# Performance work log

Hardware: AMD Instinct MI355X
Metric: run time of the kernel (lower is better)

## Reference

```python
import jax, jax.numpy as jnp
import numpy as np

N_NODES = 50000
N_EDGES = 500000
D_FEAT = 128


def setup_inputs() -> dict:
    key = jax.random.key(0)
    k1, k2, k3 = jax.random.split(key, 3)
    r = jax.random.normal(k1, (N_NODES, D_FEAT), dtype=jnp.float32)
    e = jax.random.normal(k2, (N_EDGES, D_FEAT), dtype=jnp.float32)
    a = jax.random.randint(k3, (N_EDGES, 2), 0, N_NODES, dtype=jnp.int64)
    return {"r": r, "e": e, "a": a}


def reference(r, e, a):
    # message: gather source/target node features along edges, scale by edge feats
    rij = r[a[:, 0]] * e  # [E, D] messages src -> dst
    rji = r[a[:, 1]] * e  # [E, D] messages dst -> src
    # aggregate: scatter_add into node dimension (fixed num_segments for jit)
    out = jax.ops.segment_sum(rij, a[:, 1], num_segments=r.shape[0])
    out = out + jax.ops.segment_sum(rji, a[:, 0], num_segments=r.shape[0])
    return out  # [N, D]
```

## Files before the change

kernel.cpp:

```cpp
#include <hip/hip_runtime.h>
#include <hip/hip_fp16.h>


#define D_FEAT 128
#define SCAN_TILE 1024

__device__ inline unsigned pack_h2(float a, float b) {
    __half2 h;
    h.x = __float2half_rn(a);
    h.y = __float2half_rn(b);
    return *reinterpret_cast<unsigned*>(&h);
}
__device__ inline float2 unpack_h2(unsigned u) {
    __half2 h = *reinterpret_cast<__half2*>(&u);
    return __half22float2(h);
}

__device__ inline unsigned bf16pack2(float a, float b) {
    unsigned ua = __float_as_uint(a), ub = __float_as_uint(b);
    ua += 0x7fffu + ((ua >> 16) & 1u);
    ub += 0x7fffu + ((ub >> 16) & 1u);
    return ((ua >> 16) & 0xffffu) | (ub & 0xffff0000u);
}

__global__ void hist_kernel(const int* __restrict__ a, int* __restrict__ deg,
                            int n_elems) {
    int i = blockIdx.x * blockDim.x + threadIdx.x;
    if (i < n_elems) atomicAdd(&deg[a[i]], 1);
}

__global__ void scanA_kernel(const int* __restrict__ deg, int* __restrict__ bsum,
                             int n) {
    __shared__ int wsum[16];
    int t = threadIdx.x, lane = t & 63, w = t >> 6;
    int i = blockIdx.x * SCAN_TILE + t;
    int v = (i < n) ? deg[i] : 0;
    #pragma unroll
    for (int off = 32; off > 0; off >>= 1) v += __shfl_down(v, off, 64);
    if (lane == 0) wsum[w] = v;
    __syncthreads();
    if (t == 0) {
        int s = 0;
        #pragma unroll
        for (int k = 0; k < 16; ++k) s += wsum[k];
        bsum[blockIdx.x] = s;
    }
}

__global__ void scanB_kernel(int* __restrict__ bsum, int* __restrict__ bbase,
                             int* __restrict__ offs, int nblk, int n) {
    if (threadIdx.x == 0) {
        int run = 0;
        for (int b = 0; b < nblk; ++b) {
            bbase[b] = run;
            run += bsum[b];
        }
        offs[n] = run;
    }
}

__global__ void scanC_kernel(int* __restrict__ deg, int* __restrict__ offs,
                             const int* __restrict__ bbase, int n) {
    __shared__ int wsum[16];
    int t = threadIdx.x, lane = t & 63, w = t >> 6;
    int i = blockIdx.x * SCAN_TILE + t;
    int v = (i < n) ? deg[i] : 0;
    int x = v;
    #pragma unroll
    for (int off = 1; off < 64; off <<= 1) {
        int y = __shfl_up(x, off, 64);
        if (lane >= off) x += y;
    }
    if (lane == 63) wsum[w] = x;
    __syncthreads();
    if (w == 0 && lane < 16) {
        int s = wsum[lane];
        #pragma unroll
        for (int off = 1; off < 16; off <<= 1) {
            int y = __shfl_up(s, off, 64);
            if (lane >= off) s += y;
        }
        wsum[lane] = s;
    }
    __syncthreads();
    int wbase = (w == 0) ? 0 : wsum[w - 1];
    if (i < n) {
        int excl = x - v + wbase + bbase[blockIdx.x];
        offs[i] = excl;
        deg[i] = excl;
    }
}

__global__ __launch_bounds__(256) void msg_kernel(
    const float* __restrict__ r, const float* __restrict__ e,
    const int* __restrict__ a, int* __restrict__ cursor,
    unsigned* __restrict__ msg, int n_edges) {
    int k = blockIdx.x * 4 + (threadIdx.x >> 6);
    if (k >= n_edges) return;
    int lane = threadIdx.x & 63;
    int s = a[2 * k];
    int d = a[2 * k + 1];
    int p0 = 0, p1 = 0;
    if (lane == 0) {
        p0 = atomicAdd(&cursor[d], 1);
        p1 = atomicAdd(&cursor[s], 1);
    }
    float2 ev = *((const float2*)(e + (size_t)k * D_FEAT) + lane);
    float2 rs = *((const float2*)(r + (size_t)s * D_FEAT) + lane);
    float2 rd = *((const float2*)(r + (size_t)d * D_FEAT) + lane);
    p0 = __shfl(p0, 0, 64);
    p1 = __shfl(p1, 0, 64);
    msg[(size_t)p0 * 64 + lane] = pack_h2(ev.x * rs.x, ev.y * rs.y);
    msg[(size_t)p1 * 64 + lane] = pack_h2(ev.x * rd.x, ev.y * rd.y);
}

__global__ __launch_bounds__(256) void sum_kernel(
    const unsigned* __restrict__ msg, const int* __restrict__ offs,
    float* __restrict__ out, int n_nodes) {
    int n = blockIdx.x * 4 + (threadIdx.x >> 6);
    if (n >= n_nodes) return;
    int lane = threadIdx.x & 63;
    int start = offs[n];
    int end = offs[n + 1];
    float accx = 0.f, accy = 0.f;
    int i = start;
    for (; i + 4 <= end; i += 4) {
        unsigned u0 = msg[(size_t)(i + 0) * 64 + lane];
        unsigned u1 = msg[(size_t)(i + 1) * 64 + lane];
        unsigned u2 = msg[(size_t)(i + 2) * 64 + lane];
        unsigned u3 = msg[(size_t)(i + 3) * 64 + lane];
        float2 f0 = unpack_h2(u0);
        float2 f1 = unpack_h2(u1);
        float2 f2 = unpack_h2(u2);
        float2 f3 = unpack_h2(u3);
        accx += f0.x + f1.x + f2.x + f3.x;
        accy += f0.y + f1.y + f2.y + f3.y;
    }
    for (; i < end; ++i) {
        float2 f0 = unpack_h2(msg[(size_t)i * 64 + lane]);
        accx += f0.x;
        accy += f0.y;
    }
    float2 res;
    res.x = accx;
    res.y = accy;
    *((float2*)(out + (size_t)n * D_FEAT) + lane) = res;
}


__global__ void prep_kernel(const float* __restrict__ e,
                            const float* __restrict__ r,
                            const int* __restrict__ a,
                            uint2* __restrict__ e16,
                            uint2* __restrict__ r16,
                            int* __restrict__ deg,
                            int n_e4, int n_r4, int n_entries) {
    int gid = blockIdx.x * blockDim.x + threadIdx.x;
    if (gid < n_entries) atomicAdd(&deg[a[gid]], 1);
    if (gid < n_r4) {
        const float4 v = ((const float4*)r)[gid];
        uint2 p;
        p.x = bf16pack2(v.x, v.y);
        p.y = bf16pack2(v.z, v.w);
        r16[gid] = p;
    }
    if (gid >= n_e4) return;
    const float4 v = ((const float4*)e)[gid];
    uint2 p;
    p.x = bf16pack2(v.x, v.y);
    p.y = bf16pack2(v.z, v.w);
    e16[gid] = p;
}

__global__ void fill_kernel(const int* __restrict__ a, int* __restrict__ cursor,
                            int2* __restrict__ pl, int n_entries) {
    int k = blockIdx.x * blockDim.x + threadIdx.x;
    if (k >= n_entries) return;
    int edge = k >> 1, j = k & 1;
    int other  = a[2 * edge + j];
    int center = a[2 * edge + (j ^ 1)];
    int pos = atomicAdd(&cursor[center], 1);
    pl[pos] = make_int2(edge, other);
}

__global__ __launch_bounds__(256) void gather_kernel(
    const unsigned* __restrict__ e16, const unsigned* __restrict__ r16,
    const int* __restrict__ offs, const int2* __restrict__ pl,
    float* __restrict__ out, int n_nodes) {
    int n = blockIdx.x * 4 + (threadIdx.x >> 6);
    if (n >= n_nodes) return;
    int lane = threadIdx.x & 63;
    int start = offs[n];
    int end = offs[n + 1];
    float accx = 0.f, accy = 0.f;
    int i = start;
    for (; i + 4 <= end; i += 4) {
        int2 p0 = pl[i];
        int2 p1 = pl[i + 1];
        int2 p2 = pl[i + 2];
        int2 p3 = pl[i + 3];
        unsigned ew0 = e16[(size_t)p0.x * 64 + lane];
        unsigned rw0 = r16[(size_t)p0.y * 64 + lane];
        unsigned ew1 = e16[(size_t)p1.x * 64 + lane];
        unsigned rw1 = r16[(size_t)p1.y * 64 + lane];
        unsigned ew2 = e16[(size_t)p2.x * 64 + lane];
        unsigned rw2 = r16[(size_t)p2.y * 64 + lane];
        unsigned ew3 = e16[(size_t)p3.x * 64 + lane];
        unsigned rw3 = r16[(size_t)p3.y * 64 + lane];
        accx += __uint_as_float(ew0 << 16) * __uint_as_float(rw0 << 16);
        accy += __uint_as_float(ew0 & 0xffff0000u) * __uint_as_float(rw0 & 0xffff0000u);
        accx += __uint_as_float(ew1 << 16) * __uint_as_float(rw1 << 16);
        accy += __uint_as_float(ew1 & 0xffff0000u) * __uint_as_float(rw1 & 0xffff0000u);
        accx += __uint_as_float(ew2 << 16) * __uint_as_float(rw2 << 16);
        accy += __uint_as_float(ew2 & 0xffff0000u) * __uint_as_float(rw2 & 0xffff0000u);
        accx += __uint_as_float(ew3 << 16) * __uint_as_float(rw3 << 16);
        accy += __uint_as_float(ew3 & 0xffff0000u) * __uint_as_float(rw3 & 0xffff0000u);
    }
    for (; i < end; ++i) {
        int2 p0 = pl[i];
        unsigned ew0 = e16[(size_t)p0.x * 64 + lane];
        unsigned rw0 = r16[(size_t)p0.y * 64 + lane];
        accx += __uint_as_float(ew0 << 16) * __uint_as_float(rw0 << 16);
        accy += __uint_as_float(ew0 & 0xffff0000u) * __uint_as_float(rw0 & 0xffff0000u);
    }
    float2 res;
    res.x = accx;
    res.y = accy;
    *((float2*)(out + (size_t)n * D_FEAT) + lane) = res;
}

__global__ __launch_bounds__(256) void gather_f32_kernel(
    const float* __restrict__ r, const float* __restrict__ e,
    const int* __restrict__ offs, const int2* __restrict__ pl,
    float* __restrict__ out, int n_nodes) {
    int n = blockIdx.x * 4 + (threadIdx.x >> 6);
    if (n >= n_nodes) return;
    int lane = threadIdx.x & 63;
    int start = offs[n];
    int end = offs[n + 1];
    float accx = 0.f, accy = 0.f;
    for (int i = start; i < end; ++i) {
        int2 p0 = pl[i];
        float2 ev0 = *((const float2*)(e + (size_t)p0.x * D_FEAT) + lane);
        float2 rv0 = *((const float2*)(r + (size_t)p0.y * D_FEAT) + lane);
        accx += ev0.x * rv0.x;
        accy += ev0.y * rv0.y;
    }
    float2 res;
    res.x = accx;
    res.y = accy;
    *((float2*)(out + (size_t)n * D_FEAT) + lane) = res;
}

__global__ void mp_scatter_kernel(const float* __restrict__ r,
                                  const float* __restrict__ e,
                                  const int* __restrict__ a,
                                  float* __restrict__ out,
                                  int n_edges) {
    long long gid = (long long)blockIdx.x * blockDim.x + threadIdx.x;
    int edge = (int)(gid >> 7);
    int feat = (int)(gid & 127);
    if (edge >= n_edges) return;
    int s = a[2 * edge];
    int d = a[2 * edge + 1];
    float ev = e[(long long)edge * D_FEAT + feat];
    float rs = r[(long long)s * D_FEAT + feat];
    float rd = r[(long long)d * D_FEAT + feat];
    atomicAdd(&out[(long long)d * D_FEAT + feat], rs * ev);
    atomicAdd(&out[(long long)s * D_FEAT + feat], rd * ev);
}

extern "C" void kernel_launch(void* const* d_in, const int* in_sizes, int n_in,
                              void* d_out, int out_size, void* d_ws, size_t ws_size,
                              hipStream_t stream) {
    const float* r = (const float*)d_in[0];
    const float* e = (const float*)d_in[1];
    const int*   a = (const int*)d_in[2];
    float* out = (float*)d_out;

    int n_nodes   = in_sizes[0] / D_FEAT;
    int n_edges   = in_sizes[1] / D_FEAT;
    int n_entries = 2 * n_edges;
    int n_e4      = in_sizes[1] / 4;
    int n_r4      = in_sizes[0] / 4;

    int block = 256;
    int grid_e = (n_entries + block - 1) / block;
    int nblk_scan = (n_nodes + SCAN_TILE - 1) / SCAN_TILE;

    {
        size_t ints_head = (size_t)n_nodes + (size_t)(n_nodes + 1)
                         + 2 * (size_t)nblk_scan;
        ints_head = (ints_head + 63) & ~(size_t)63;
        size_t need = ints_head * sizeof(int)
                    + (size_t)n_entries * 64 * sizeof(unsigned);
        if (ws_size >= need && nblk_scan <= 1024) {
            int* deg   = (int*)d_ws;
            int* offs  = deg + n_nodes;
            int* bsum  = offs + n_nodes + 1;
            int* bbase = bsum + nblk_scan;
            unsigned* msg = (unsigned*)((int*)d_ws + ints_head);

            hipMemsetAsync(deg, 0, (size_t)n_nodes * sizeof(int), stream);
            hist_kernel<<<grid_e, block, 0, stream>>>(a, deg, n_entries);
            scanA_kernel<<<nblk_scan, SCAN_TILE, 0, stream>>>(deg, bsum, n_nodes);
            scanB_kernel<<<1, 64, 0, stream>>>(bsum, bbase, offs, nblk_scan,
                                               n_nodes);
            scanC_kernel<<<nblk_scan, SCAN_TILE, 0, stream>>>(deg, offs, bbase,
                                                              n_nodes);
            int grid_m = (n_edges + 3) / 4;
            msg_kernel<<<grid_m, 256, 0, stream>>>(r, e, a, deg, msg, n_edges);
            int grid_g = (n_nodes + 3) / 4;
            sum_kernel<<<grid_g, 256, 0, stream>>>(msg, offs, out, n_nodes);
            return;
        }
    }

    {
        size_t ints_head = (size_t)n_nodes + (size_t)(n_nodes + 1)
                         + 2 * (size_t)nblk_scan;
        ints_head = (ints_head + 1) & ~(size_t)1;
        size_t need = ((size_t)n_e4 + (size_t)n_r4) * sizeof(uint2)
                    + ints_head * sizeof(int)
                    + (size_t)n_entries * sizeof(int2);
        if (ws_size >= need && nblk_scan <= 1024) {
            uint2* e16  = (uint2*)d_ws;
            uint2* r16  = e16 + n_e4;
            int*   deg  = (int*)(r16 + n_r4);
            int*   offs = deg + n_nodes;
            int*   bsum = offs + n_nodes + 1;
            int*   bbase= bsum + nblk_scan;
            int2*  pl   = (int2*)((int*)(r16 + n_r4) + ints_head);

            hipMemsetAsync(deg, 0, (size_t)n_nodes * sizeof(int), stream);
            int grid_p = (n_e4 + block - 1) / block;
            prep_kernel<<<grid_p, block, 0, stream>>>(e, r, a, e16, r16, deg,
                                                      n_e4, n_r4, n_entries);
            scanA_kernel<<<nblk_scan, SCAN_TILE, 0, stream>>>(deg, bsum, n_nodes);
            scanB_kernel<<<1, 64, 0, stream>>>(bsum, bbase, offs, nblk_scan,
                                               n_nodes);
            scanC_kernel<<<nblk_scan, SCAN_TILE, 0, stream>>>(deg, offs, bbase,
                                                              n_nodes);
            fill_kernel<<<grid_e, block, 0, stream>>>(a, deg, pl, n_entries);
            int grid_g = (n_nodes + 3) / 4;
            gather_kernel<<<grid_g, 256, 0, stream>>>(
                (const unsigned*)e16, (const unsigned*)r16, offs, pl, out,
                n_nodes);
            return;
        }
    }

    {
        size_t ints_head = (size_t)n_nodes + (size_t)(n_nodes + 1)
                         + 2 * (size_t)nblk_scan;
        ints_head = (ints_head + 1) & ~(size_t)1;
        size_t need = ints_head * sizeof(int) + (size_t)n_entries * sizeof(int2);
        if (ws_size >= need && nblk_scan <= 1024) {
            int*  deg  = (int*)d_ws;
            int*  offs = deg + n_nodes;
            int*  bsum = offs + n_nodes + 1;
            int*  bbase= bsum + nblk_scan;
            int2* pl   = (int2*)((int*)d_ws + ints_head);

            hipMemsetAsync(deg, 0, (size_t)n_nodes * sizeof(int), stream);
            hist_kernel<<<grid_e, block, 0, stream>>>(a, deg, n_entries);
            scanA_kernel<<<nblk_scan, SCAN_TILE, 0, stream>>>(deg, bsum, n_nodes);
            scanB_kernel<<<1, 64, 0, stream>>>(bsum, bbase, offs, nblk_scan,
                                               n_nodes);
            scanC_kernel<<<nblk_scan, SCAN_TILE, 0, stream>>>(deg, offs, bbase,
                                                              n_nodes);
            fill_kernel<<<grid_e, block, 0, stream>>>(a, deg, pl, n_entries);
            int grid_g = (n_nodes + 3) / 4;
            gather_f32_kernel<<<grid_g, 256, 0, stream>>>(r, e, offs, pl, out,
                                                          n_nodes);
            return;
        }
    }

    hipMemsetAsync(d_out, 0, (size_t)out_size * sizeof(float), stream);
    long long total = (long long)n_edges * D_FEAT;
    long long grid = (total + block - 1) / block;
    mp_scatter_kernel<<<(int)grid, block, 0, stream>>>(r, e, a, out, n_edges);
}
```

Baseline: 596.3 us.

## Write messages in edge order with permutation list and fp16 node copy

The message kernel now writes each message contiguously at its edge-ordered slot rather than scattering it to a CSR position, and records the slot in a permutation array that the sum kernel uses for an indirect gather. Node features are converted to fp16 in a prep kernel that is fused with the degree histogram, which halves the bytes of the random node-row reads. Scattered writes become coalesced, but the sum kernel gains an extra index indirection and random reads, and the node features lose precision.

```diff
diff --git a/kernel.cpp b/kernel.cpp
--- a/kernel.cpp
+++ b/kernel.cpp
@@ -21,6 +21,21 @@
     ua += 0x7fffu + ((ua >> 16) & 1u);
     ub += 0x7fffu + ((ub >> 16) & 1u);
     return ((ua >> 16) & 0xffffu) | (ub & 0xffff0000u);
+}
+
+__global__ void prep_r_kernel(const float* __restrict__ r,
+                              const int* __restrict__ a,
+                              uint2* __restrict__ r16,
+                              int* __restrict__ deg,
+                              int n_r4, int n_entries) {
+    int gid = blockIdx.x * blockDim.x + threadIdx.x;
+    if (gid < n_entries) atomicAdd(&deg[a[gid]], 1);
+    if (gid >= n_r4) return;
+    const float4 v = ((const float4*)r)[gid];
+    uint2 p;
+    p.x = pack_h2(v.x, v.y);
+    p.y = pack_h2(v.z, v.w);
+    r16[gid] = p;
 }
 
 __global__ void hist_kernel(const int* __restrict__ a, int* __restrict__ deg,
@@ -91,32 +106,31 @@
     }
 }
 
-__global__ __launch_bounds__(256) void msg_kernel(
-    const float* __restrict__ r, const float* __restrict__ e,
+__global__ __launch_bounds__(256) void msg2_kernel(
+    const unsigned* __restrict__ r16, const float* __restrict__ e,
     const int* __restrict__ a, int* __restrict__ cursor,
-    unsigned* __restrict__ msg, int n_edges) {
+    int* __restrict__ plm, unsigned* __restrict__ msg, int n_edges) {
     int k = blockIdx.x * 4 + (threadIdx.x >> 6);
     if (k >= n_edges) return;
     int lane = threadIdx.x & 63;
     int s = a[2 * k];
     int d = a[2 * k + 1];
-    int p0 = 0, p1 = 0;
     if (lane == 0) {
-        p0 = atomicAdd(&cursor[d], 1);
-        p1 = atomicAdd(&cursor[s], 1);
+        int p0 = atomicAdd(&cursor[d], 1);
+        int p1 = atomicAdd(&cursor[s], 1);
+        plm[p0] = 2 * k;
+        plm[p1] = 2 * k + 1;
     }
     float2 ev = *((const float2*)(e + (size_t)k * D_FEAT) + lane);
-    float2 rs = *((const float2*)(r + (size_t)s * D_FEAT) + lane);
-    float2 rd = *((const float2*)(r + (size_t)d * D_FEAT) + lane);
-    p0 = __shfl(p0, 0, 64);
-    p1 = __shfl(p1, 0, 64);
-    msg[(size_t)p0 * 64 + lane] = pack_h2(ev.x * rs.x, ev.y * rs.y);
-    msg[(size_t)p1 * 64 + lane] = pack_h2(ev.x * rd.x, ev.y * rd.y);
-}
-
-__global__ __launch_bounds__(256) void sum_kernel(
+    float2 rs = unpack_h2(r16[(size_t)s * 64 + lane]);
+    float2 rd = unpack_h2(r16[(size_t)d * 64 + lane]);
+    msg[(size_t)(2 * k) * 64 + lane]     = pack_h2(ev.x * rs.x, ev.y * rs.y);
+    msg[(size_t)(2 * k + 1) * 64 + lane] = pack_h2(ev.x * rd.x, ev.y * rd.y);
+}
+
+__global__ __launch_bounds__(256) void sum2_kernel(
     const unsigned* __restrict__ msg, const int* __restrict__ offs,
-    float* __restrict__ out, int n_nodes) {
+    const int* __restrict__ plm, float* __restrict__ out, int n_nodes) {
     int n = blockIdx.x * 4 + (threadIdx.x >> 6);
     if (n >= n_nodes) return;
     int lane = threadIdx.x & 63;
@@ -125,10 +139,14 @@
     float accx = 0.f, accy = 0.f;
     int i = start;
     for (; i + 4 <= end; i += 4) {
-        unsigned u0 = msg[(size_t)(i + 0) * 64 + lane];
-        unsigned u1 = msg[(size_t)(i + 1) * 64 + lane];
-        unsigned u2 = msg[(size_t)(i + 2) * 64 + lane];
-        unsigned u3 = msg[(size_t)(i + 3) * 64 + lane];
+        int m0 = plm[i];
+        int m1 = plm[i + 1];
+        int m2 = plm[i + 2];
+        int m3 = plm[i + 3];
+        unsigned u0 = msg[(size_t)m0 * 64 + lane];
+        unsigned u1 = msg[(size_t)m1 * 64 + lane];
+        unsigned u2 = msg[(size_t)m2 * 64 + lane];
+        unsigned u3 = msg[(size_t)m3 * 64 + lane];
         float2 f0 = unpack_h2(u0);
         float2 f1 = unpack_h2(u1);
         float2 f2 = unpack_h2(u2);
@@ -137,7 +155,7 @@
         accy += f0.y + f1.y + f2.y + f3.y;
     }
     for (; i < end; ++i) {
-        float2 f0 = unpack_h2(msg[(size_t)i * 64 + lane]);
+        float2 f0 = unpack_h2(msg[(size_t)plm[i] * 64 + lane]);
         accx += f0.x;
         accy += f0.y;
     }
@@ -290,28 +308,36 @@
 
     {
         size_t ints_head = (size_t)n_nodes + (size_t)(n_nodes + 1)
-                         + 2 * (size_t)nblk_scan;
+                         + 2 * (size_t)nblk_scan + (size_t)n_entries;
         ints_head = (ints_head + 63) & ~(size_t)63;
-        size_t need = ints_head * sizeof(int)
+        size_t need = (size_t)n_r4 * sizeof(uint2)
+                    + ints_head * sizeof(int)
                     + (size_t)n_entries * 64 * sizeof(unsigned);
         if (ws_size >= need && nblk_scan <= 1024) {
-            int* deg   = (int*)d_ws;
+            uint2* r16 = (uint2*)d_ws;
+            int* deg   = (int*)(r16 + n_r4);
             int* offs  = deg + n_nodes;
             int* bsum  = offs + n_nodes + 1;
             int* bbase = bsum + nblk_scan;
-            unsigned* msg = (unsigned*)((int*)d_ws + ints_head);
+            int* plm   = bbase + nblk_scan;
+            unsigned* msg = (unsigned*)((int*)(r16 + n_r4) + ints_head);
 
             hipMemsetAsync(deg, 0, (size_t)n_nodes * sizeof(int), stream);
-            hist_kernel<<<grid_e, block, 0, stream>>>(a, deg, n_entries);
+            int grid_p = (n_r4 + block - 1) / block;
+            if (grid_p < grid_e) grid_p = grid_e;
+            prep_r_kernel<<<grid_p, block, 0, stream>>>(r, a, r16, deg,
+                                                        n_r4, n_entries);
             scanA_kernel<<<nblk_scan, SCAN_TILE, 0, stream>>>(deg, bsum, n_nodes);
             scanB_kernel<<<1, 64, 0, stream>>>(bsum, bbase, offs, nblk_scan,
                                                n_nodes);
             scanC_kernel<<<nblk_scan, SCAN_TILE, 0, stream>>>(deg, offs, bbase,
                                                               n_nodes);
             int grid_m = (n_edges + 3) / 4;
-            msg_kernel<<<grid_m, 256, 0, stream>>>(r, e, a, deg, msg, n_edges);
+            msg2_kernel<<<grid_m, 256, 0, stream>>>((const unsigned*)r16, e, a,
+                                                    deg, plm, msg, n_edges);
             int grid_g = (n_nodes + 3) / 4;
-            sum_kernel<<<grid_g, 256, 0, stream>>>(msg, offs, out, n_nodes);
+            sum2_kernel<<<grid_g, 256, 0, stream>>>(msg, offs, plm, out,
+                                                    n_nodes);
             return;
         }
     }
```

New measurement: 586.4 us. Within noise of the previous version (-1.7%).
